# Kernel optimization log

Measured on AMD Instinct MI355X. Metric: run time of the kernel, lower is better.

The kernel has to match this reference:

```python
import jax, jax.numpy as jnp
import numpy as np

STATE_DIM = 100   # nx*ny = 20*5
HIDDEN = 8        # BlackBox(8)
N_OBS = 12
T = 65536
DT = 0.01


def setup_inputs() -> dict:
    key = jax.random.key(0)
    ks = jax.random.split(key, 10)
    c0 = jax.random.normal(ks[0], (STATE_DIM,), dtype=jnp.float32)
    w = jax.random.normal(ks[1], (T, 2), dtype=jnp.float32)
    u = 0.1 * jax.random.normal(ks[2], (T, STATE_DIM), dtype=jnp.float32)
    # Stable transition matrix: contraction + small random coupling
    A = (0.9 * jnp.eye(STATE_DIM, dtype=jnp.float32)
         + 0.01 * jax.random.normal(ks[3], (STATE_DIM, STATE_DIM), dtype=jnp.float32))
    Bw = 0.1 * jax.random.normal(ks[4], (STATE_DIM, 2), dtype=jnp.float32)
    W1 = jax.random.normal(ks[5], (HIDDEN, STATE_DIM), dtype=jnp.float32) / jnp.sqrt(STATE_DIM).astype(jnp.float32)
    b1 = jnp.zeros((HIDDEN,), dtype=jnp.float32)
    W2 = jax.random.normal(ks[6], (STATE_DIM, HIDDEN), dtype=jnp.float32) / jnp.sqrt(HIDDEN).astype(jnp.float32)
    b2 = jnp.zeros((STATE_DIM,), dtype=jnp.float32)
    obs_idx = jax.random.randint(ks[7], (N_OBS,), 0, STATE_DIM, dtype=jnp.int32)
    return {"c0": c0, "w": w, "u": u, "A": A, "Bw": Bw,
            "W1": W1, "b1": b1, "W2": W2, "b2": b2, "obs_idx": obs_idx}


def reference(c0, w, u, A, Bw, W1, b1, W2, b2, obs_idx):
    """Grey-box rollout:
    f_t = BlackBox(c_{t-1}) = W2 @ tanh(W1 @ c + b1) + b2
    c_t = WhiteBox(c_{t-1}, w_t, u_t, f_t) = A@c + Bw@w_t + u_t + dt*f_t
    y_t = c_t[obs_idx]
    Returns (c, y) with shapes (T, STATE_DIM), (T, N_OBS).
    """
    def step(c, xs):
        wt, ut = xs
        f = W2 @ jnp.tanh(W1 @ c + b1) + b2          # black box correction
        c_next = A @ c + Bw @ wt + ut + DT * f       # white box physics step
        return c_next, (c_next, c_next[obs_idx])

    _, (c, y) = jax.lax.scan(step, c0, (w, u))
    return c, y
```

## Files before the change

### kernel.cpp

```cpp
#include <hip/hip_runtime.h>
#include <math.h>


#define T_STEPS 65536
#define SD 100
#define DT_F 0.01f

__device__ __forceinline__ float dpp_xor1_add(float x) {
  int v = __builtin_amdgcn_update_dpp(0, __float_as_int(x), 0xB1, 0xF, 0xF, true);
  return x + __int_as_float(v);
}
template <int PAT>
__device__ __forceinline__ float dppq(float x) {
  return __int_as_float(__builtin_amdgcn_update_dpp(0, __float_as_int(x), PAT, 0xF, 0xF, true));
}
__device__ __forceinline__ float tanh_fast(float x) {
  float e = __builtin_amdgcn_exp2f(x * 2.885390081777927f);
  return 1.f - 2.f * __builtin_amdgcn_rcpf(e + 1.f);
}
__device__ __forceinline__ float rdlane(float v, int l) {
  return __int_as_float(__builtin_amdgcn_readlane(__float_as_int(v), l));
}

__global__ __launch_bounds__(256, 1) void k0_setup(
    const float* __restrict__ A, const float* __restrict__ W1,
    const float* __restrict__ W2, float* __restrict__ A8o,
    float* __restrict__ A256o, float* __restrict__ Pws,
    float* __restrict__ Gws, float* __restrict__ Qws) {
  __shared__ __align__(16) float Al[10000];
  __shared__ __align__(16) float M0[10000];
  __shared__ __align__(16) float M1[10000];
  __shared__ __align__(16) float Pb[2][800];
  __shared__ __align__(16) float Vb[2][800];
  const int tid = threadIdx.x;
  for (int i = tid; i < 2500; i += 256) {
    ((float4*)Al)[i] = ((const float4*)A)[i];
    ((float4*)M0)[i] = ((const float4*)A)[i];
  }
  __syncthreads();
  for (int s = 0; s < 8; ++s) {
    const float* src = (s & 1) ? M1 : M0;
    float* dst = (s & 1) ? M0 : M1;
    if (tid < 100) {
      float4 acc[25];
      #pragma unroll
      for (int i = 0; i < 25; ++i) acc[i] = make_float4(0.f, 0.f, 0.f, 0.f);
      for (int k = 0; k < 100; ++k) {
        float a = src[tid * 100 + k];
        const float4* rk = (const float4*)(src + k * 100);
        #pragma unroll
        for (int i = 0; i < 25; ++i) {
          float4 r4 = rk[i];
          acc[i].x = fmaf(a, r4.x, acc[i].x);
          acc[i].y = fmaf(a, r4.y, acc[i].y);
          acc[i].z = fmaf(a, r4.z, acc[i].z);
          acc[i].w = fmaf(a, r4.w, acc[i].w);
        }
      }
      #pragma unroll
      for (int i = 0; i < 25; ++i) ((float4*)(dst + tid * 100))[i] = acc[i];
    }
    __syncthreads();
    if (s == 2) for (int i = tid; i < 2500; i += 256) ((float4*)A8o)[i] = ((const float4*)dst)[i];
    if (s == 7) for (int i = tid; i < 2500; i += 256) ((float4*)A256o)[i] = ((const float4*)dst)[i];
    __syncthreads();
  }
  for (int i = tid; i < 800; i += 256) Pb[0][i] = W1[i];
  __syncthreads();
  for (int k = 0; k < 24; ++k) {
    const float* Pc = Pb[k & 1];
    if (k <= 22 && tid < 64) {
      int i = tid >> 3, c = tid & 7;
      float g = 0.f;
      for (int l = 0; l < 100; ++l) g = fmaf(Pc[i * 100 + l], W2[l * 8 + c], g);
      Gws[k * 64 + i * 8 + c] = DT_F * g;
    }
    if (k >= 16) for (int i = tid; i < 800; i += 256) Pws[(k - 16) * 800 + i] = DT_F * Pc[i];
    __syncthreads();
    if (k < 23) {
      float* Pn = Pb[(k + 1) & 1];
      if (tid < 64) {
        int i = tid >> 3, cg = tid & 7;
        int c0 = cg * 13, c1 = c0 + 13 < 100 ? c0 + 13 : 100;
        for (int c = c0; c < c1; ++c) {
          float v = 0.f;
          for (int l = 0; l < 100; ++l) v = fmaf(Pc[i * 100 + l], Al[l * 100 + c], v);
          Pn[i * 100 + c] = v;
        }
      }
    }
    __syncthreads();
  }
  for (int i = tid; i < 800; i += 256) Vb[0][i] = W2[i];
  __syncthreads();
  for (int j = 0; j < 8; ++j) {
    const float* Vc = Vb[j & 1];
    for (int i = tid; i < 800; i += 256) Qws[(7 - j) * 800 + i] = Vc[i];
    __syncthreads();
    if (j < 7 && tid < 100) {
      float acc[8];
      #pragma unroll
      for (int c = 0; c < 8; ++c) acc[c] = 0.f;
      for (int l = 0; l < 100; ++l) {
        float av = Al[tid * 100 + l];
        #pragma unroll
        for (int c = 0; c < 8; ++c) acc[c] = fmaf(av, Vc[l * 8 + c], acc[c]);
      }
      float* dst = Vb[(j + 1) & 1] + tid * 8;
      #pragma unroll
      for (int c = 0; c < 8; ++c) dst[c] = acc[c];
    }
    __syncthreads();
  }
}

template <int MODE>
__global__ __launch_bounds__(256, 1) void k_rollout(
    const float* __restrict__ Amat, const float* __restrict__ Bw,
    const float* __restrict__ b2v, const float* __restrict__ ug,
    const float* __restrict__ wg, const float* __restrict__ W2,
    const float* __restrict__ hbufg, const float* __restrict__ W1,
    const float* __restrict__ b1v, const float* __restrict__ c0,
    const float* __restrict__ Xin, float* __restrict__ SendOut,
    float* __restrict__ Lc, float* __restrict__ qbuf,
    const int* __restrict__ obs, float* __restrict__ out_y) {
  __shared__ __align__(16) float cc[64 * 100];
  __shared__ __align__(16) float uc[64 * 100];
  __shared__ __align__(16) float wc[64 * 2];
  __shared__ __align__(16) float hc[64 * 8];
  __shared__ float W1l[800];
  __shared__ float b1l[8];
  __shared__ int obsl[12];
  const int tid = threadIdx.x;
  const int blk = blockIdx.x;
  const int base = blk * 256;
  const int row = tid >> 1, half = tid & 1;
  float aW[52];
  float w2h0 = 0.f, w2h1 = 0.f, w2h2 = 0.f, w2h3 = 0.f;
  float bw0 = 0.f, bw1 = 0.f, cst = 0.f;
  if (tid < 200) {
    #pragma unroll
    for (int j = 0; j < 52; ++j) {
      int col = half * 48 + j;
      bool valid = half ? (j >= 2) : (j < 50);
      aW[j] = valid ? Amat[row * SD + col] : 0.f;
    }
    if (MODE >= 2) {
      w2h0 = W2[row * 8 + half * 4 + 0];
      w2h1 = W2[row * 8 + half * 4 + 1];
      w2h2 = W2[row * 8 + half * 4 + 2];
      w2h3 = W2[row * 8 + half * 4 + 3];
    } else if (half == 0) {
      bw0 = Bw[row * 2 + 0];
      bw1 = Bw[row * 2 + 1];
      cst = DT_F * b2v[row];
    }
  }
  if (MODE == 1) {
    for (int i = tid; i < 800; i += 256) W1l[i] = W1[i];
    if (tid < 8) b1l[tid] = b1v[tid];
  }
  if (MODE == 3 && tid < 12) obsl[tid] = obs[tid];
  if (tid < SD) {
    float v = 0.f;
    if (MODE == 1 || MODE == 3) v = Xin[blk * SD + tid];
    cc[63 * SD + tid] = v;
  }
  if (MODE == 1 && blk == 0 && tid < 8) {
    float q0 = b1v[tid];
    for (int l = 0; l < SD; ++l) q0 = fmaf(W1[tid * SD + l], c0[l], q0);
    qbuf[tid] = q0;
  }

  for (int kk = 0; kk < 4; ++kk) {
    __syncthreads();
    if (MODE < 2) {
      const float* us = ug + (size_t)(base + kk * 64) * SD;
      for (int i = tid; i < 1600; i += 256) ((float4*)uc)[i] = ((const float4*)us)[i];
      if (tid < 128) wc[tid] = wg[(size_t)(base + kk * 64) * 2 + tid];
    } else {
      const float* hs = hbufg + (size_t)(base + kk * 64) * 8;
      for (int i = tid; i < 128; i += 256) ((float4*)hc)[i] = ((const float4*)hs)[i];
    }
    for (int t = 0; t < 64; ++t) {
      __syncthreads();
      const float* cprev = cc + ((t + 63) & 63) * SD;
      if (tid < 200) {
        const float4* cb = (const float4*)cprev + half * 12;
        float p0 = 0.f, p1 = 0.f, p2 = 0.f, p3 = 0.f;
        #pragma unroll
        for (int i = 0; i < 13; ++i) {
          float4 c4 = cb[i];
          p0 = fmaf(aW[4 * i + 0], c4.x, p0);
          p1 = fmaf(aW[4 * i + 1], c4.y, p1);
          p2 = fmaf(aW[4 * i + 2], c4.z, p2);
          p3 = fmaf(aW[4 * i + 3], c4.w, p3);
        }
        float acc = (p0 + p1) + (p2 + p3);
        if (MODE >= 2) {
          float4 h4 = *(const float4*)(hc + t * 8 + half * 4);
          acc = fmaf(w2h0, h4.x, acc);
          acc = fmaf(w2h1, h4.y, acc);
          acc = fmaf(w2h2, h4.z, acc);
          acc = fmaf(w2h3, h4.w, acc);
        } else if (half == 0) {
          float2 wv = *(const float2*)(wc + t * 2);
          acc += cst + bw0 * wv.x + bw1 * wv.y + uc[t * SD + row];
        }
        acc = dpp_xor1_add(acc);
        if (half == 0) cc[t * SD + row] = acc;
      }
    }
    __syncthreads();
    if (MODE == 1) {
      float4* Ld = (float4*)(Lc + (size_t)(base + kk * 64) * SD);
      for (int i = tid; i < 1600; i += 256) Ld[i] = ((const float4*)cc)[i];
      for (int e = tid; e < 512; e += 256) {
        int sl = e >> 3, zr = e & 7;
        float qv = b1l[zr];
        const float4* crow = (const float4*)(cc + sl * SD);
        const float* wr = W1l + zr * SD;
        #pragma unroll
        for (int i = 0; i < 25; ++i) {
          float4 c4 = crow[i];
          qv = fmaf(wr[4 * i + 0], c4.x, qv);
          qv = fmaf(wr[4 * i + 1], c4.y, qv);
          qv = fmaf(wr[4 * i + 2], c4.z, qv);
          qv = fmaf(wr[4 * i + 3], c4.w, qv);
        }
        qbuf[(size_t)(base + kk * 64 + sl + 1) * 8 + zr] = qv;
      }
    } else if (MODE == 3) {
      for (int e = tid; e < 768; e += 256) {
        int sl = e / 12, j = e - sl * 12;
        int tg = base + kk * 64 + sl;
        out_y[(size_t)tg * 12 + j] =
            Lc[(size_t)tg * SD + obsl[j]] + DT_F * cc[sl * SD + obsl[j]];
      }
      __syncthreads();
      float4* Ld = (float4*)(Lc + (size_t)(base + kk * 64) * SD);
      for (int i = tid; i < 1600; i += 256) {
        float4 L4 = Ld[i];
        float4 r4 = ((const float4*)cc)[i];
        L4.x = fmaf(DT_F, r4.x, L4.x);
        L4.y = fmaf(DT_F, r4.y, L4.y);
        L4.z = fmaf(DT_F, r4.z, L4.z);
        L4.w = fmaf(DT_F, r4.w, L4.w);
        Ld[i] = L4;
      }
    }
  }
  if (MODE == 0 || MODE == 2) {
    __syncthreads();
    if (tid < 25)
      ((float4*)(SendOut + blk * SD))[tid] = ((const float4*)(cc + 63 * SD))[tid];
  }
}

__global__ __launch_bounds__(256, 1) void k_scan(
    const float* __restrict__ A256, const float* __restrict__ Send,
    const float* __restrict__ c0, int use_c0, float* __restrict__ Xout) {
  __shared__ __align__(16) float X[256][100];
  __shared__ __align__(16) float sc[64 * 100];
  const int tid = threadIdx.x;
  const int row = tid >> 1, half = tid & 1;
  float aW[52];
  if (tid < 200) {
    #pragma unroll
    for (int j = 0; j < 52; ++j) {
      int col = half * 48 + j;
      bool valid = half ? (j >= 2) : (j < 50);
      aW[j] = valid ? A256[row * SD + col] : 0.f;
    }
  }
  if (tid < SD) X[0][tid] = use_c0 ? c0[tid] : 0.f;
  for (int b = 0; b < 255; ++b) {
    if ((b & 63) == 0) {
      __syncthreads();
      for (int i = tid; i < 1600; i += 256)
        ((float4*)sc)[i] = ((const float4*)(Send + b * SD))[i];
    }
    __syncthreads();
    if (tid < 200) {
      const float4* cb = (const float4*)(&X[b][0]) + half * 12;
      float p0 = 0.f, p1 = 0.f, p2 = 0.f, p3 = 0.f;
      #pragma unroll
      for (int i = 0; i < 13; ++i) {
        float4 c4 = cb[i];
        p0 = fmaf(aW[4 * i + 0], c4.x, p0);
        p1 = fmaf(aW[4 * i + 1], c4.y, p1);
        p2 = fmaf(aW[4 * i + 2], c4.z, p2);
        p3 = fmaf(aW[4 * i + 3], c4.w, p3);
      }
      float acc = (p0 + p1) + (p2 + p3);
      if (half == 0) acc += sc[(b & 63) * SD + row];
      acc = dpp_xor1_add(acc);
      if (half == 0) X[b + 1][row] = acc;
    }
  }
  __syncthreads();
  for (int i = tid; i < 6400; i += 256) ((float4*)Xout)[i] = ((const float4*)X)[i];
}

#define QSTEP(BASE, TT)                                                       \
  {                                                                           \
    const int SL = (BASE) + (TT);                                             \
    if (lane < 16) {                                                          \
      float za = G0p[0] * cur;                                                \
      za = fmaf(G0p[1], dppq<0xB1>(cur), za);                                 \
      za = fmaf(G0p[2], dppq<0x4E>(cur), za);                                 \
      za = fmaf(G0p[3], dppq<0x1B>(cur), za);                                 \
      float vx4 = dppq<0x124>(cur);                                           \
      za = fmaf(G0p[4], vx4, za);                                             \
      za = fmaf(G0p[5], dppq<0xB1>(vx4), za);                                 \
      za = fmaf(G0p[6], dppq<0x4E>(vx4), za);                                 \
      za = fmaf(G0p[7], dppq<0x1B>(vx4), za);                                 \
      za += zbv[TT];                                                          \
      za += zpP[(TT) & 1];                                                    \
      cur = tanh_fast(za);                                                    \
      hring[SL * 8 + l7] = cur;                                               \
    }                                                                         \
    const float h0 = rdlane(cur, 0), h1 = rdlane(cur, 1);                     \
    const float h2 = rdlane(cur, 2), h3 = rdlane(cur, 3);                     \
    const float h4 = rdlane(cur, 4), h5 = rdlane(cur, 5);                     \
    const float h6 = rdlane(cur, 6), h7 = rdlane(cur, 7);                     \
    if (lane >= 8) {                                                          \
      float acc = s2s[((TT) + 1) & 7];                                        \
      acc = fmaf(GcA[0], h0, acc); acc = fmaf(GcA[1], h1, acc);               \
      acc = fmaf(GcA[2], h2, acc); acc = fmaf(GcA[3], h3, acc);               \
      acc = fmaf(GcA[4], h4, acc); acc = fmaf(GcA[5], h5, acc);               \
      acc = fmaf(GcA[6], h6, acc); acc = fmaf(GcA[7], h7, acc);               \
      float sB = GcB[0] * h0;                                                 \
      sB = fmaf(GcB[1], h1, sB); sB = fmaf(GcB[2], h2, sB);                   \
      sB = fmaf(GcB[3], h3, sB); sB = fmaf(GcB[4], h4, sB);                   \
      sB = fmaf(GcB[5], h5, sB); sB = fmaf(GcB[6], h6, sB);                   \
      sB = fmaf(GcB[7], h7, sB);                                              \
      acc += chainpre;                                                        \
      s2s[(TT) & 7] = sB;                                                     \
      *(float*)((char*)zacc + addrW[SL]) = acc;                               \
      chainpre = *(const float*)((char*)zacc + addrR[SL]);                    \
    }                                                                         \
    if (lane < 16) {                                                          \
      zpP[(TT) & 1] = zacc[((SL + 2) & 15) * 8 + l7];                         \
      if ((TT) < 6) zbv[(TT) + 2] = basep[((SL + 2) & 15) * 8 + l7];          \
    }                                                                         \
  }

#define K4_HALF(BASE, DOFLUSH)                                                \
  {                                                                           \
    if (lane < 16) {                                                          \
      zbv[0] = basep[(BASE)*8 + l7];                                          \
      zbv[1] = basep[((BASE) + 1) * 8 + l7];                                  \
    }                                                                         \
    if (DOFLUSH) {                                                            \
      if (lane < 4) {                                                         \
        const float* fsrc = hring + ((BASE) ? 0 : 64) + lane * 16;            \
        float4* fdst = (float4*)(hflush + lane * 16);                         \
        fdst[0] = *(const float4*)(fsrc);                                     \
        fdst[1] = *(const float4*)(fsrc + 4);                                 \
        fdst[2] = *(const float4*)(fsrc + 8);                                 \
        fdst[3] = *(const float4*)(fsrc + 12);                                \
      }                                                                       \
      hflush += 64;                                                           \
    }                                                                         \
    QSTEP(BASE, 0) QSTEP(BASE, 1) QSTEP(BASE, 2) QSTEP(BASE, 3)               \
    QSTEP(BASE, 4) QSTEP(BASE, 5) QSTEP(BASE, 6) QSTEP(BASE, 7)               \
    __syncthreads();                                                          \
  }

__global__ __launch_bounds__(256, 1) void k4_core(
    const float* __restrict__ qbuf, const float* __restrict__ A8w,
    const float* __restrict__ Pws, const float* __restrict__ Gws,
    const float* __restrict__ Qws, float* __restrict__ hbuf,
    unsigned int* flagp) {
  const int tid = threadIdx.x;

  if (blockIdx.x != 0) {
    if (tid < 64) {
      float x0 = 1.f, x1 = 1.f, x2 = 1.f, x3 = 1.f;
      for (int it = 0; it < 1000000; ++it) {
        #pragma unroll
        for (int j = 0; j < 8; ++j) {
          x0 = fmaf(x0, 1.0000001f, 1e-33f);
          x1 = fmaf(x1, 0.9999999f, 1e-33f);
          x2 = fmaf(x2, 1.0000002f, 1e-33f);
          x3 = fmaf(x3, 0.9999998f, 1e-33f);
        }
        if ((it & 3) == 0) {
          if (__hip_atomic_load(flagp, __ATOMIC_RELAXED,
                                __HIP_MEMORY_SCOPE_AGENT) != 0u)
            break;
        }
      }
      asm volatile("" ::"v"(x0), "v"(x1), "v"(x2), "v"(x3));
    }
    return;
  }

  __shared__ __align__(16) float zacc[16 * 8 + 8];
  __shared__ __align__(16) float basep[16 * 8];
  __shared__ __align__(16) float hring[16 * 8];
  __shared__ __align__(16) float rbuf[2][100];
  const int wave = tid >> 6;
  const int lane = tid & 63;

  for (int i = tid; i < 136; i += 256) zacc[i] = 0.f;
  for (int i = tid; i < 128; i += 256) hring[i] = 0.f;
  if (tid < 200) ((float*)rbuf)[tid] = 0.f;

  if (wave == 0) {
    const int l7 = lane & 7;
    const int g = (lane >> 3) - 1;
    const int ci = lane & 7;
    float G0p[8];
    float GcA[8], GcB[8];
    int addrW[16], addrR[16];
    if (lane < 16) {
      #pragma unroll
      for (int o = 0; o < 8; ++o) G0p[o] = Gws[l7 * 8 + (l7 ^ o)];
    }
    if (lane >= 8) {
      const int kA = 1 + g;
      const int kB = 8 + g;
      #pragma unroll
      for (int c = 0; c < 8; ++c) {
        GcA[c] = Gws[kA * 64 + ci * 8 + c];
        GcB[c] = Gws[kB * 64 + ci * 8 + c];
      }
      #pragma unroll
      for (int k = 0; k < 16; ++k)
        addrW[k] = (((k + 2 + g) & 15) * 8 + ci) * 4;
      #pragma unroll
      for (int k = 0; k < 16; ++k)
        addrR[k] = (g == 6) ? (128 + ci) * 4 : addrW[(k + 1) & 15];
    }
    __syncthreads();

    float cur = 0.f, chainpre = 0.f;
    float zpP[2];
    float zbv[8];
    float s2s[8];
    zpP[0] = 0.f;
    zpP[1] = 0.f;
    #pragma unroll
    for (int j = 0; j < 8; ++j) { zbv[j] = 0.f; s2s[j] = 0.f; }
    float* hflush = hbuf;

    K4_HALF(0, 0)
    K4_HALF(8, 1)
    for (int mm = 1; mm < 4096; ++mm) {
      K4_HALF(0, 1)
      K4_HALF(8, 1)
    }
    if (lane < 4) {
      const float* fsrc = hring + 64 + lane * 16;
      float4* fdst = (float4*)(hflush + lane * 16);
      fdst[0] = *(const float4*)(fsrc);
      fdst[1] = *(const float4*)(fsrc + 4);
      fdst[2] = *(const float4*)(fsrc + 8);
      fdst[3] = *(const float4*)(fsrc + 12);
    }
  } else if (wave == 1 || wave == 3) {
    const int rrow = (wave == 1) ? lane : 64 + lane;
    float A8row[100];
    float Qrow[64];
    if (rrow < 100) {
      #pragma unroll
      for (int i = 0; i < 25; ++i)
        *(float4*)&A8row[4 * i] = ((const float4*)(A8w + rrow * 100))[i];
      #pragma unroll
      for (int i = 0; i < 8; ++i)
        #pragma unroll
        for (int c = 0; c < 8; ++c) Qrow[i * 8 + c] = Qws[i * 800 + rrow * 8 + c];
    }
    __syncthreads();
    for (int m = 0; m < 8192; ++m) {
      if (rrow < 100) {
        const float* rp = rbuf[(m + 1) & 1];
        float p0 = 0.f, p1 = 0.f, p2 = 0.f, p3 = 0.f;
        #pragma unroll
        for (int i = 0; i < 25; ++i) {
          float4 r4 = ((const float4*)rp)[i];
          p0 = fmaf(A8row[4 * i + 0], r4.x, p0);
          p1 = fmaf(A8row[4 * i + 1], r4.y, p1);
          p2 = fmaf(A8row[4 * i + 2], r4.z, p2);
          p3 = fmaf(A8row[4 * i + 3], r4.w, p3);
        }
        const float* hb = hring + ((m - 1) & 1) * 64;
        float q0 = 0.f, q1 = 0.f, q2 = 0.f, q3 = 0.f;
        #pragma unroll
        for (int i = 0; i < 8; ++i) {
          float4 x0 = *(const float4*)(hb + i * 8);
          float4 x1 = *(const float4*)(hb + i * 8 + 4);
          q0 = fmaf(Qrow[i * 8 + 0], x0.x, q0);
          q1 = fmaf(Qrow[i * 8 + 1], x0.y, q1);
          q2 = fmaf(Qrow[i * 8 + 2], x0.z, q2);
          q3 = fmaf(Qrow[i * 8 + 3], x0.w, q3);
          q0 = fmaf(Qrow[i * 8 + 4], x1.x, q0);
          q1 = fmaf(Qrow[i * 8 + 5], x1.y, q1);
          q2 = fmaf(Qrow[i * 8 + 6], x1.z, q2);
          q3 = fmaf(Qrow[i * 8 + 7], x1.w, q3);
        }
        rbuf[m & 1][rrow] = ((p0 + p1) + (p2 + p3)) + ((q0 + q1) + (q2 + q3));
      }
      __syncthreads();
    }
  } else {
    const int wj = lane >> 3, wi = lane & 7;
    float Prow[100];
    float Gw2[64];
    #pragma unroll
    for (int i = 0; i < 25; ++i)
      *(float4*)&Prow[4 * i] = ((const float4*)(Pws + wj * 800 + wi * 100))[i];
    #pragma unroll
    for (int jj = 0; jj < 8; ++jj)
      #pragma unroll
      for (int c = 0; c < 8; ++c)
        Gw2[jj * 8 + c] =
            (jj > wj) ? 0.f : Gws[(15 + wj - jj) * 64 + wi * 8 + c];
    float qpipe[4];
    #pragma unroll
    for (int i = 0; i < 4; ++i)
      qpipe[i] = qbuf[(size_t)((i + 1) * 8 + wj) * 8 + wi];
    basep[wj * 8 + wi] = qbuf[wj * 8 + wi];
    __syncthreads();
    for (int mo = 0; mo < 2048; ++mo) {
      #pragma unroll
      for (int mi = 0; mi < 4; ++mi) {
        const int m = mo * 4 + mi;
        float qv = qpipe[mi];
        int mp = m + 5;
        if (mp > 8192) mp = 8192;
        qpipe[mi] = qbuf[(size_t)(mp * 8 + wj) * 8 + wi];
        const float* rp = rbuf[(mi + 1) & 1];
        float p0 = 0.f, p1 = 0.f, p2 = 0.f, p3 = 0.f;
        #pragma unroll
        for (int i = 0; i < 25; ++i) {
          float4 r4 = ((const float4*)rp)[i];
          p0 = fmaf(Prow[4 * i + 0], r4.x, p0);
          p1 = fmaf(Prow[4 * i + 1], r4.y, p1);
          p2 = fmaf(Prow[4 * i + 2], r4.z, p2);
          p3 = fmaf(Prow[4 * i + 3], r4.w, p3);
        }
        const float* hb = hring + ((mi + 1) & 1) * 64;
        float g0 = 0.f, g1 = 0.f, g2 = 0.f, g3 = 0.f;
        #pragma unroll
        for (int jj = 0; jj < 8; ++jj) {
          float4 x0 = *(const float4*)(hb + jj * 8);
          float4 x1 = *(const float4*)(hb + jj * 8 + 4);
          g0 = fmaf(Gw2[jj * 8 + 0], x0.x, g0);
          g1 = fmaf(Gw2[jj * 8 + 1], x0.y, g1);
          g2 = fmaf(Gw2[jj * 8 + 2], x0.z, g2);
          g3 = fmaf(Gw2[jj * 8 + 3], x0.w, g3);
          g0 = fmaf(Gw2[jj * 8 + 4], x1.x, g0);
          g1 = fmaf(Gw2[jj * 8 + 5], x1.y, g1);
          g2 = fmaf(Gw2[jj * 8 + 6], x1.z, g2);
          g3 = fmaf(Gw2[jj * 8 + 7], x1.w, g3);
        }
        basep[(((mi + 1) & 1) * 8 + wj) * 8 + wi] =
            qv + ((p0 + p1) + (p2 + p3)) + ((g0 + g1) + (g2 + g3));
        __syncthreads();
      }
    }
  }

  __syncthreads();
  if (tid == 0)
    __hip_atomic_store(flagp, 1u, __ATOMIC_RELAXED, __HIP_MEMORY_SCOPE_AGENT);
}

extern "C" void kernel_launch(void* const* d_in, const int* in_sizes, int n_in,
                              void* d_out, int out_size, void* d_ws, size_t ws_size,
                              hipStream_t stream) {
  const float* c0 = (const float*)d_in[0];
  const float* w  = (const float*)d_in[1];
  const float* u  = (const float*)d_in[2];
  const float* A  = (const float*)d_in[3];
  const float* Bw = (const float*)d_in[4];
  const float* W1 = (const float*)d_in[5];
  const float* b1 = (const float*)d_in[6];
  const float* W2 = (const float*)d_in[7];
  const float* b2 = (const float*)d_in[8];
  const int* obs  = (const int*)d_in[9];
  float* out_c = (float*)d_out;
  float* out_y = out_c + (size_t)T_STEPS * SD;

  float* wsf = (float*)d_ws;
  float* A8    = wsf;
  float* A256  = wsf + 10000;
  float* Pws   = wsf + 20000;
  float* Gws   = wsf + 26400;
  float* Qws   = wsf + 27872;
  float* Send  = wsf + 34272;
  float* X     = wsf + 59872;
  float* qbuf  = wsf + 85472;
  float* hbuf  = wsf + 609888;
  float* SendR = wsf + 1134240;
  float* XR    = wsf + 1159840;

  hipLaunchKernelGGL(k0_setup, dim3(1), dim3(256), 0, stream,
                     A, W1, W2, A8, A256, Pws, Gws, Qws);
  hipLaunchKernelGGL(k_rollout<0>, dim3(256), dim3(256), 0, stream,
                     A, Bw, b2, u, w, (const float*)nullptr, (const float*)nullptr,
                     (const float*)nullptr, (const float*)nullptr, (const float*)nullptr,
                     (const float*)nullptr, Send, (float*)nullptr, (float*)nullptr,
                     (const int*)nullptr, (float*)nullptr);
  hipLaunchKernelGGL(k_scan, dim3(1), dim3(256), 0, stream, A256, Send, c0, 1, X);
  hipLaunchKernelGGL(k_rollout<1>, dim3(256), dim3(256), 0, stream,
                     A, Bw, b2, u, w, (const float*)nullptr, (const float*)nullptr,
                     W1, b1, c0, X, (float*)nullptr, out_c, qbuf,
                     (const int*)nullptr, (float*)nullptr);
  hipMemsetAsync(Send, 0, sizeof(unsigned int), stream);
  hipLaunchKernelGGL(k4_core, dim3(256), dim3(256), 0, stream,
                     qbuf, A8, Pws, Gws, Qws, hbuf, (unsigned int*)Send);
  hipLaunchKernelGGL(k_rollout<2>, dim3(256), dim3(256), 0, stream,
                     A, (const float*)nullptr, (const float*)nullptr,
                     (const float*)nullptr, (const float*)nullptr, W2, hbuf,
                     (const float*)nullptr, (const float*)nullptr, (const float*)nullptr,
                     (const float*)nullptr, SendR, (float*)nullptr, (float*)nullptr,
                     (const int*)nullptr, (float*)nullptr);
  hipLaunchKernelGGL(k_scan, dim3(1), dim3(256), 0, stream, A256, SendR,
                     (const float*)nullptr, 0, XR);
  hipLaunchKernelGGL(k_rollout<3>, dim3(256), dim3(256), 0, stream,
                     A, (const float*)nullptr, (const float*)nullptr,
                     (const float*)nullptr, (const float*)nullptr, W2, hbuf,
                     (const float*)nullptr, (const float*)nullptr, (const float*)nullptr,
                     XR, (float*)nullptr, out_c, (float*)nullptr, obs, out_y);
}
```

Baseline: 13.22 ms.

## Defer GcB products to next step and raise core wave priority

The serial recurrence step is reorganized so the sB partial sum for the B-group is computed from the previous step's hidden values, held in a register double buffer, before the tanh chain starts. This takes those eight FMAs off the critical path between tanh and the zacc store. The bias add is folded into the first FMA of the za chain. The core wave now gets raised scheduling priority. The spinning filler blocks use all threads with 8 independent FMA chains and a large unused LDS allocation, apparently to control clocks and occupancy. That adds power draw and register pressure in return.

```diff
diff --git a/kernel.cpp b/kernel.cpp
--- a/kernel.cpp
+++ b/kernel.cpp
@@ -305,8 +305,19 @@
 #define QSTEP(BASE, TT)                                                       \
   {                                                                           \
     const int SL = (BASE) + (TT);                                             \
+    float sB = 0.f, seedC = 0.f;                                              \
+    if (lane >= 8) {                                                          \
+      const float* hp = hs[((TT) + 1) & 1];                                   \
+      sB = GcB[0] * hp[0];                                                    \
+      sB = fmaf(GcB[1], hp[1], sB); sB = fmaf(GcB[2], hp[2], sB);             \
+      sB = fmaf(GcB[3], hp[3], sB); sB = fmaf(GcB[4], hp[4], sB);             \
+      sB = fmaf(GcB[5], hp[5], sB); sB = fmaf(GcB[6], hp[6], sB);             \
+      sB = fmaf(GcB[7], hp[7], sB);                                           \
+      seedC = chainpre + s2s[((TT) + 2) & 7];                                 \
+    }                                                                         \
     if (lane < 16) {                                                          \
-      float za = G0p[0] * cur;                                                \
+      float zs = zbv[TT] + zpP[(TT) & 1];                                     \
+      float za = fmaf(G0p[0], cur, zs);                                       \
       za = fmaf(G0p[1], dppq<0xB1>(cur), za);                                 \
       za = fmaf(G0p[2], dppq<0x4E>(cur), za);                                 \
       za = fmaf(G0p[3], dppq<0x1B>(cur), za);                                 \
@@ -315,30 +326,25 @@
       za = fmaf(G0p[5], dppq<0xB1>(vx4), za);                                 \
       za = fmaf(G0p[6], dppq<0x4E>(vx4), za);                                 \
       za = fmaf(G0p[7], dppq<0x1B>(vx4), za);                                 \
-      za += zbv[TT];                                                          \
-      za += zpP[(TT) & 1];                                                    \
       cur = tanh_fast(za);                                                    \
       hring[SL * 8 + l7] = cur;                                               \
     }                                                                         \
-    const float h0 = rdlane(cur, 0), h1 = rdlane(cur, 1);                     \
-    const float h2 = rdlane(cur, 2), h3 = rdlane(cur, 3);                     \
-    const float h4 = rdlane(cur, 4), h5 = rdlane(cur, 5);                     \
-    const float h6 = rdlane(cur, 6), h7 = rdlane(cur, 7);                     \
-    if (lane >= 8) {                                                          \
-      float acc = s2s[((TT) + 1) & 7];                                        \
-      acc = fmaf(GcA[0], h0, acc); acc = fmaf(GcA[1], h1, acc);               \
-      acc = fmaf(GcA[2], h2, acc); acc = fmaf(GcA[3], h3, acc);               \
-      acc = fmaf(GcA[4], h4, acc); acc = fmaf(GcA[5], h5, acc);               \
-      acc = fmaf(GcA[6], h6, acc); acc = fmaf(GcA[7], h7, acc);               \
-      float sB = GcB[0] * h0;                                                 \
-      sB = fmaf(GcB[1], h1, sB); sB = fmaf(GcB[2], h2, sB);                   \
-      sB = fmaf(GcB[3], h3, sB); sB = fmaf(GcB[4], h4, sB);                   \
-      sB = fmaf(GcB[5], h5, sB); sB = fmaf(GcB[6], h6, sB);                   \
-      sB = fmaf(GcB[7], h7, sB);                                              \
-      acc += chainpre;                                                        \
-      s2s[(TT) & 7] = sB;                                                     \
-      *(float*)((char*)zacc + addrW[SL]) = acc;                               \
-      chainpre = *(const float*)((char*)zacc + addrR[SL]);                    \
+    {                                                                         \
+      float* hn = hs[(TT) & 1];                                               \
+      hn[0] = rdlane(cur, 0); hn[1] = rdlane(cur, 1);                         \
+      hn[2] = rdlane(cur, 2); hn[3] = rdlane(cur, 3);                         \
+      hn[4] = rdlane(cur, 4); hn[5] = rdlane(cur, 5);                         \
+      hn[6] = rdlane(cur, 6); hn[7] = rdlane(cur, 7);                         \
+      if (lane >= 8) {                                                        \
+        float acc = fmaf(GcA[0], hn[0], seedC);                               \
+        acc = fmaf(GcA[1], hn[1], acc); acc = fmaf(GcA[2], hn[2], acc);       \
+        acc = fmaf(GcA[3], hn[3], acc); acc = fmaf(GcA[4], hn[4], acc);       \
+        acc = fmaf(GcA[5], hn[5], acc); acc = fmaf(GcA[6], hn[6], acc);       \
+        acc = fmaf(GcA[7], hn[7], acc);                                       \
+        s2s[(TT) & 7] = sB;                                                   \
+        *(float*)((char*)zacc + addrW[SL]) = acc;                             \
+        chainpre = *(const float*)((char*)zacc + addrR[SL]);                  \
+      }                                                                       \
     }                                                                         \
     if (lane < 16) {                                                          \
       zpP[(TT) & 1] = zacc[((SL + 2) & 15) * 8 + l7];                         \
@@ -374,26 +380,32 @@
     const float* __restrict__ Qws, float* __restrict__ hbuf,
     unsigned int* flagp) {
   const int tid = threadIdx.x;
+  __shared__ float lds_guard[20480];
+  if (flagp == (unsigned int*)0) lds_guard[tid] = 1.f;
 
   if (blockIdx.x != 0) {
-    if (tid < 64) {
-      float x0 = 1.f, x1 = 1.f, x2 = 1.f, x3 = 1.f;
-      for (int it = 0; it < 1000000; ++it) {
-        #pragma unroll
-        for (int j = 0; j < 8; ++j) {
-          x0 = fmaf(x0, 1.0000001f, 1e-33f);
-          x1 = fmaf(x1, 0.9999999f, 1e-33f);
-          x2 = fmaf(x2, 1.0000002f, 1e-33f);
-          x3 = fmaf(x3, 0.9999998f, 1e-33f);
-        }
-        if ((it & 3) == 0) {
-          if (__hip_atomic_load(flagp, __ATOMIC_RELAXED,
-                                __HIP_MEMORY_SCOPE_AGENT) != 0u)
-            break;
-        }
-      }
-      asm volatile("" ::"v"(x0), "v"(x1), "v"(x2), "v"(x3));
-    }
+    float x0 = 1.f, x1 = 1.01f, x2 = 1.02f, x3 = 1.03f;
+    float x4 = 1.04f, x5 = 1.05f, x6 = 1.06f, x7 = 1.07f;
+    for (int it = 0; it < 600000; ++it) {
+      #pragma unroll
+      for (int j = 0; j < 4; ++j) {
+        x0 = fmaf(x0, 1.0000001f, 1e-30f);
+        x1 = fmaf(x1, 0.9999999f, 1e-30f);
+        x2 = fmaf(x2, 1.0000002f, 1e-30f);
+        x3 = fmaf(x3, 0.9999998f, 1e-30f);
+        x4 = fmaf(x4, 1.0000003f, 1e-30f);
+        x5 = fmaf(x5, 0.9999997f, 1e-30f);
+        x6 = fmaf(x6, 1.0000004f, 1e-30f);
+        x7 = fmaf(x7, 0.9999996f, 1e-30f);
+      }
+      if ((it & 63) == 0) {
+        if (__hip_atomic_load(flagp, __ATOMIC_RELAXED,
+                              __HIP_MEMORY_SCOPE_AGENT) != 0u)
+          break;
+      }
+    }
+    asm volatile("" ::"v"(x0), "v"(x1), "v"(x2), "v"(x3), "v"(x4), "v"(x5),
+                 "v"(x6), "v"(x7));
     return;
   }
 
@@ -409,6 +421,7 @@
   if (tid < 200) ((float*)rbuf)[tid] = 0.f;
 
   if (wave == 0) {
+    __builtin_amdgcn_s_setprio(1);
     const int l7 = lane & 7;
     const int g = (lane >> 3) - 1;
     const int ci = lane & 7;
@@ -440,10 +453,13 @@
     float zpP[2];
     float zbv[8];
     float s2s[8];
+    float hs[2][8];
     zpP[0] = 0.f;
     zpP[1] = 0.f;
     #pragma unroll
-    for (int j = 0; j < 8; ++j) { zbv[j] = 0.f; s2s[j] = 0.f; }
+    for (int j = 0; j < 8; ++j) {
+      zbv[j] = 0.f; s2s[j] = 0.f; hs[0][j] = 0.f; hs[1][j] = 0.f;
+    }
     float* hflush = hbuf;
 
     K4_HALF(0, 0)
```

Result: faster. 12.88 ms (-2.5%).
